# Optimization experiments

Measured on AMD Instinct MI355X. Metric: run time of the kernel, lower is better.

## Reference

```python
import jax, jax.numpy as jnp
import numpy as np

B, S, D = 2, 2048, 2048
H = 16
HD = D // H  # 128

def setup_inputs() -> dict:
    key = jax.random.key(0)
    k1, k2, k3 = jax.random.split(key, 3)
    x = jax.random.normal(k1, (B, S, D), dtype=jnp.float32)
    w_qkv = jax.random.normal(k2, (D, 3 * D), dtype=jnp.float32) * (1.0 / np.sqrt(D))
    b_qkv = jnp.zeros((3 * D,), dtype=jnp.float32)
    w_out = jax.random.normal(k3, (D, D), dtype=jnp.float32) * (1.0 / np.sqrt(D))
    b_out = jnp.zeros((D,), dtype=jnp.float32)
    return {"x": x, "w_qkv": w_qkv, "b_qkv": b_qkv, "w_out": w_out, "b_out": b_out}

def reference(x, w_qkv, b_qkv, w_out, b_out):
    batch, seq_len, channels = x.shape
    qkv = x @ w_qkv + b_qkv                      # [B,S,3D]
    q, k, v = jnp.split(qkv, 3, axis=-1)
    # [B,S,D] -> [B,H,S,HD]
    def heads(t):
        return t.reshape(batch, seq_len, H, HD).transpose(0, 2, 1, 3)
    q, k, v = heads(q), heads(k), heads(v)
    scale = 1.0 / np.sqrt(HD).astype(np.float32)
    attn = jnp.einsum('bhqd,bhkd->bhqk', q, k) * scale
    causal = jnp.tril(jnp.ones((seq_len, seq_len), dtype=bool))
    attn = jnp.where(causal, attn, -jnp.inf)
    attn = jax.nn.softmax(attn, axis=-1)
    y = jnp.einsum('bhqk,bhkd->bhqd', attn, v)   # [B,H,S,HD]
    y = y.transpose(0, 2, 1, 3).reshape(batch, seq_len, channels)
    return y @ w_out + b_out
```

## Files before the change

### kernel.cpp

```cpp
#include <hip/hip_runtime.h>
#include <hip/hip_bf16.h>
#include <cstdint>
#include <cstddef>

#define BB 2
#define SS 2048
#define DD 2048
#define HH 16
#define HDIM 128
#define QSCALE 0.12751743f

typedef short bf16x8 __attribute__((ext_vector_type(8)));
typedef float f32x4 __attribute__((ext_vector_type(4)));
typedef float f32x16 __attribute__((ext_vector_type(16)));

__device__ __forceinline__ ushort f2bf(float f) {
    union { float f; uint32_t u; } v; v.f = f;
    uint32_t u = v.u;
    u += 0x7fffu + ((u >> 16) & 1u);
    return (ushort)(u >> 16);
}

__device__ __forceinline__ ushort f2bf_fast(float f) {
    union { float f; uint32_t u; } v; v.f = f;
    return (ushort)((v.u + 0x8000u) >> 16);
}

__device__ __forceinline__ void gl16(const ushort* g, ushort* l) {
    __builtin_amdgcn_global_load_lds(
        (const __attribute__((address_space(1))) unsigned int*)g,
        (__attribute__((address_space(3))) unsigned int*)l,
        16, 0, 0);
}

__global__ __launch_bounds__(256) void cast_x_kernel(
    const float* __restrict__ X, ushort* __restrict__ Xb)
{
    size_t idx = ((size_t)blockIdx.x * 256 + threadIdx.x) * 8;
    float4 a = *(const float4*)(X + idx);
    float4 b = *(const float4*)(X + idx + 4);
    ushort4 o0, o1;
    o0.x = f2bf(a.x); o0.y = f2bf(a.y); o0.z = f2bf(a.z); o0.w = f2bf(a.w);
    o1.x = f2bf(b.x); o1.y = f2bf(b.y); o1.z = f2bf(b.z); o1.w = f2bf(b.w);
    *(ushort4*)(Xb + idx) = o0;
    *(ushort4*)(Xb + idx + 4) = o1;
}

__global__ __launch_bounds__(256) void transpose_cast_kernel(
    const float* __restrict__ W, ushort* __restrict__ Wt, int K, int N)
{
    __shared__ ushort tile[32][36];
    const int n0 = blockIdx.x * 32;
    const int k0 = blockIdx.y * 32;
    const int t = threadIdx.x;
    const int r = t >> 3;
    const int c = (t & 7) * 4;
    float4 a = *(const float4*)(W + (size_t)(k0 + r) * N + n0 + c);
    tile[r][c + 0] = f2bf(a.x); tile[r][c + 1] = f2bf(a.y);
    tile[r][c + 2] = f2bf(a.z); tile[r][c + 3] = f2bf(a.w);
    __syncthreads();
    ushort4 o;
    o.x = tile[c + 0][r]; o.y = tile[c + 1][r];
    o.z = tile[c + 2][r]; o.w = tile[c + 3][r];
    *(ushort4*)(Wt + (size_t)(n0 + r) * K + k0 + c) = o;
}

__global__ __launch_bounds__(256) void transpose_v_kernel(
    const ushort* __restrict__ V, ushort* __restrict__ Vt)
{
    __shared__ ushort tile[32][36];
    const int s0 = blockIdx.x * 32;
    const int h0 = blockIdx.y * 32;
    const int bh = blockIdx.z;
    const ushort* Vp = V + (size_t)bh * SS * HDIM;
    ushort* Vtp = Vt + (size_t)bh * HDIM * SS;
    const int t = threadIdx.x;
    const int r = t >> 3;
    const int c = (t & 7) * 4;
    *(ushort4*)&tile[r][c] = *(const ushort4*)(Vp + (size_t)(s0 + r) * HDIM + h0 + c);
    __syncthreads();
    ushort4 o;
    o.x = tile[c + 0][r]; o.y = tile[c + 1][r];
    o.z = tile[c + 2][r]; o.w = tile[c + 3][r];
    *(ushort4*)(Vtp + (size_t)(h0 + r) * SS + s0 + c) = o;
}

#define NTK 32

__global__ __launch_bounds__(512) void gemm_qkv_kernel(
    const ushort* __restrict__ A, const ushort* __restrict__ Bt,
    const float* __restrict__ bias,
    ushort* __restrict__ Qo, ushort* __restrict__ Ko, ushort* __restrict__ Vo)
{
    const int bid = blockIdx.x;
    const int wgid = (bid & 7) * 48 + (bid >> 3);
    const int mt = wgid / 24;
    const int nt = wgid - mt * 24;
    const int m0 = mt * 256, n0 = nt * 256;

    __shared__ ushort As[2][2][8192];
    __shared__ ushort Bs[2][2][8192];

    const int tid = threadIdx.x;
    const int w = tid >> 6, lane = tid & 63;
    const int wr = w >> 2, wc = w & 3;
    const int l15 = lane & 15, l4x = lane >> 4, l7 = lane & 7;

    const int rt  = w * 8 + (lane >> 3);
    const int giA = (lane & 7) ^ (lane >> 3);
    const size_t aoff = (size_t)(m0 + rt) * DD + giA * 8;
    const int nb = (w >> 2) * 64 + (w & 3) * 8 + (lane >> 3);
    const size_t boff = (size_t)(n0 + nb) * DD + giA * 8;
    const int ldst = w * 512;

    const int rdA = (wr * 64 + l15) << 7;
    const int rdB = (wc * 32 + l15) << 7;
    const int cb0 = (l4x ^ l7) << 4;
    const int cb1 = ((l4x ^ l7) ^ 4) << 4;

#define STAGE_A(t, qm) do { \
    gl16(A + aoff + (size_t)((qm) * 64) * DD + (t) * 64,       &As[(t) & 1][qm][ldst]); \
    gl16(A + aoff + (size_t)(128 + (qm) * 64) * DD + (t) * 64, &As[(t) & 1][qm][4096 + ldst]); \
} while (0)
#define STAGE_B(t, qn) do { \
    gl16(Bt + boff + (size_t)((qn) * 32) * DD + (t) * 64,       &Bs[(t) & 1][qn][ldst]); \
    gl16(Bt + boff + (size_t)(128 + (qn) * 32) * DD + (t) * 64, &Bs[(t) & 1][qn][4096 + ldst]); \
} while (0)
#define MFMA(d, x, y) d = __builtin_amdgcn_mfma_f32_16x16x32_bf16(x, y, d, 0, 0, 0)

    f32x4 acc[8][4];
#pragma unroll
    for (int i = 0; i < 8; ++i)
#pragma unroll
        for (int j = 0; j < 4; ++j) acc[i][j] = (f32x4)0.f;

    bf16x8 a[4][2], b0[2][2], b1[2][2];

    STAGE_A(0, 0); STAGE_B(0, 1); STAGE_B(0, 0); STAGE_A(0, 1);
    STAGE_A(1, 0); STAGE_B(1, 1);
    asm volatile("s_waitcnt vmcnt(4)" ::: "memory");
    __builtin_amdgcn_s_barrier();

#pragma unroll 1
    for (int t = 0; t < NTK; ++t) {
        const char* Ab = (const char*)As + (t & 1) * 32768;
        const char* Bb = (const char*)Bs + (t & 1) * 32768;

#pragma unroll
        for (int mf = 0; mf < 4; ++mf) {
            a[mf][0] = *(const bf16x8*)(Ab + rdA + mf * 2048 + cb0);
            a[mf][1] = *(const bf16x8*)(Ab + rdA + mf * 2048 + cb1);
        }
#pragma unroll
        for (int nf = 0; nf < 2; ++nf) {
            b0[nf][0] = *(const bf16x8*)(Bb + rdB + nf * 2048 + cb0);
            b0[nf][1] = *(const bf16x8*)(Bb + rdB + nf * 2048 + cb1);
        }
        if (t + 1 < NTK) STAGE_B(t + 1, 0);
        __builtin_amdgcn_s_barrier();
        asm volatile("s_waitcnt lgkmcnt(0)" ::: "memory");
        __builtin_amdgcn_s_setprio(1);
#pragma unroll
        for (int mf = 0; mf < 4; ++mf)
#pragma unroll
            for (int nf = 0; nf < 2; ++nf) {
                MFMA(acc[mf][nf], a[mf][0], b0[nf][0]);
                MFMA(acc[mf][nf], a[mf][1], b0[nf][1]);
            }
        __builtin_amdgcn_s_setprio(0);
        __builtin_amdgcn_s_barrier();

#pragma unroll
        for (int nf = 0; nf < 2; ++nf) {
            b1[nf][0] = *(const bf16x8*)(Bb + 16384 + rdB + nf * 2048 + cb0);
            b1[nf][1] = *(const bf16x8*)(Bb + 16384 + rdB + nf * 2048 + cb1);
        }
        if (t + 1 < NTK) STAGE_A(t + 1, 1);
        __builtin_amdgcn_s_barrier();
        asm volatile("s_waitcnt lgkmcnt(0)" ::: "memory");
        __builtin_amdgcn_s_setprio(1);
#pragma unroll
        for (int mf = 0; mf < 4; ++mf)
#pragma unroll
            for (int nf = 0; nf < 2; ++nf) {
                MFMA(acc[mf][2 + nf], a[mf][0], b1[nf][0]);
                MFMA(acc[mf][2 + nf], a[mf][1], b1[nf][1]);
            }
        __builtin_amdgcn_s_setprio(0);
        __builtin_amdgcn_s_barrier();

#pragma unroll
        for (int mf = 0; mf < 4; ++mf) {
            a[mf][0] = *(const bf16x8*)(Ab + 16384 + rdA + mf * 2048 + cb0);
            a[mf][1] = *(const bf16x8*)(Ab + 16384 + rdA + mf * 2048 + cb1);
        }
        if (t + 2 < NTK) STAGE_A(t + 2, 0);
        __builtin_amdgcn_s_barrier();
        asm volatile("s_waitcnt lgkmcnt(0)" ::: "memory");
        __builtin_amdgcn_s_setprio(1);
#pragma unroll
        for (int mf = 0; mf < 4; ++mf)
#pragma unroll
            for (int nf = 0; nf < 2; ++nf) {
                MFMA(acc[4 + mf][2 + nf], a[mf][0], b1[nf][0]);
                MFMA(acc[4 + mf][2 + nf], a[mf][1], b1[nf][1]);
            }
        __builtin_amdgcn_s_setprio(0);
        __builtin_amdgcn_s_barrier();

        if (t + 2 < NTK) STAGE_B(t + 2, 1);
        __builtin_amdgcn_s_barrier();
        __builtin_amdgcn_s_setprio(1);
#pragma unroll
        for (int mf = 0; mf < 4; ++mf)
#pragma unroll
            for (int nf = 0; nf < 2; ++nf) {
                MFMA(acc[4 + mf][nf], a[mf][0], b0[nf][0]);
                MFMA(acc[4 + mf][nf], a[mf][1], b0[nf][1]);
            }
        __builtin_amdgcn_s_setprio(0);
        if (t + 2 < NTK)      { asm volatile("s_waitcnt vmcnt(4)" ::: "memory"); }
        else if (t + 1 < NTK) { asm volatile("s_waitcnt vmcnt(0)" ::: "memory"); }
        __builtin_amdgcn_s_barrier();
    }
#undef STAGE_A
#undef STAGE_B
#undef MFMA

    const int which = n0 >> 11;
    ushort* dst = (which == 0) ? Qo : ((which == 1) ? Ko : Vo);
    const float sc = (which == 0) ? QSCALE : 1.0f;
    const int bidx = m0 >> 11;
    const int srow = (m0 & 2047) + wr * 128 + l4x * 4;
#pragma unroll
    for (int NF = 0; NF < 4; ++NF) {
        int n = n0 + wc * 64 + NF * 16 + l15;
        int cch = n & 2047;
        int h = cch >> 7, hd = cch & 127;
        float bv = bias[n];
        size_t base = ((size_t)(bidx * HH + h) * SS) * HDIM + hd;
#pragma unroll
        for (int MF = 0; MF < 8; ++MF) {
#pragma unroll
            for (int r = 0; r < 4; ++r) {
                int s = srow + MF * 16 + r;
                dst[base + (size_t)s * HDIM] = f2bf((acc[MF][NF][r] + bv) * sc);
            }
        }
    }
}

__global__ __launch_bounds__(256) void gemm_out_kernel(
    const ushort* __restrict__ A, const ushort* __restrict__ Bt,
    const float* __restrict__ bias, float* __restrict__ Out)
{
    const int n0 = blockIdx.x * 128;
    const int m0 = blockIdx.y * 128;
    __shared__ ushort As[128 * 32];
    __shared__ ushort Bs[128 * 32];
    const int t = threadIdx.x, w = t >> 6, lane = t & 63;
    const int l31 = lane & 31, hh = lane >> 5;
    const int lrow = lane >> 2, lks = lane & 3;
    const int wr = w >> 1, wc = w & 1;
    const int swst = (lrow >> 1) & 3;
    const int swr  = (l31 >> 1) & 3;

    f32x16 acc[2][2];
#pragma unroll
    for (int i = 0; i < 2; ++i)
#pragma unroll
        for (int j = 0; j < 2; ++j) acc[i][j] = (f32x16)0.f;

    for (int k0 = 0; k0 < DD; k0 += 32) {
        __syncthreads();
#pragma unroll
        for (int q = 0; q < 2; ++q) {
            int e = w * 2 + q;
            int row = e * 16 + lrow;
            gl16(A  + (size_t)(m0 + row) * DD + k0 + (lks ^ swst) * 8, &As[e * 512]);
            gl16(Bt + (size_t)(n0 + row) * DD + k0 + (lks ^ swst) * 8, &Bs[e * 512]);
        }
        __syncthreads();
#pragma unroll
        for (int k16 = 0; k16 < 2; ++k16) {
            int co = ((k16 * 2 + hh) ^ swr) * 8;
            bf16x8 ar0 = *(const bf16x8*)&As[(wr * 64 + l31) * 32 + co];
            bf16x8 ar1 = *(const bf16x8*)&As[(wr * 64 + 32 + l31) * 32 + co];
            bf16x8 br0 = *(const bf16x8*)&Bs[(wc * 64 + l31) * 32 + co];
            bf16x8 br1 = *(const bf16x8*)&Bs[(wc * 64 + 32 + l31) * 32 + co];
            acc[0][0] = __builtin_amdgcn_mfma_f32_32x32x16_bf16(ar0, br0, acc[0][0], 0, 0, 0);
            acc[0][1] = __builtin_amdgcn_mfma_f32_32x32x16_bf16(ar0, br1, acc[0][1], 0, 0, 0);
            acc[1][0] = __builtin_amdgcn_mfma_f32_32x32x16_bf16(ar1, br0, acc[1][0], 0, 0, 0);
            acc[1][1] = __builtin_amdgcn_mfma_f32_32x32x16_bf16(ar1, br1, acc[1][1], 0, 0, 0);
        }
    }

#pragma unroll
    for (int j = 0; j < 2; ++j) {
        int n = n0 + wc * 64 + j * 32 + l31;
        float bv = bias[n];
#pragma unroll
        for (int i = 0; i < 2; ++i) {
#pragma unroll
            for (int r = 0; r < 16; ++r) {
                int m = m0 + wr * 64 + i * 32 + (r & 3) + 8 * (r >> 2) + 4 * hh;
                Out[(size_t)m * DD + n] = acc[i][j][r] + bv;
            }
        }
    }
}

__global__ __launch_bounds__(256, 2) void attn_mfma_kernel(
    const ushort* __restrict__ Q, const ushort* __restrict__ K,
    const ushort* __restrict__ Vt, ushort* __restrict__ Y)
{
    const int bh = blockIdx.y;
    const int qt = gridDim.x - 1 - blockIdx.x;
    const int q0 = qt * 128;
    const int b = bh >> 4, h = bh & 15;

    __shared__ ushort Ks[4 * 64 * 32];
    __shared__ ushort Vs[2 * 128 * 32];
    __shared__ ushort Ps[128 * 32];

    const int t = threadIdx.x, w = t >> 6, lane = t & 63;
    const int l31 = lane & 31, hh = lane >> 5;
    const int lrow = lane >> 2, lks = lane & 3;
    const int swst = (lrow >> 1) & 3;
    const int swr  = (l31 >> 1) & 3;

    const ushort* Qp = Q  + (size_t)bh * SS * HDIM;
    const ushort* Kp = K  + (size_t)bh * SS * HDIM;
    const ushort* Vp = Vt + (size_t)bh * HDIM * SS;

    bf16x8 aq[8];
#pragma unroll
    for (int kb2 = 0; kb2 < 8; ++kb2)
        aq[kb2] = *(const bf16x8*)(Qp + (size_t)(q0 + w * 32 + l31) * HDIM + kb2 * 16 + hh * 8);

    bf16x8 ones;
#pragma unroll
    for (int j = 0; j < 8; ++j) ones[j] = (short)0x3F80;

    f32x16 O[4];
#pragma unroll
    for (int nt = 0; nt < 4; ++nt) O[nt] = (f32x16)0.f;
    f32x16 Ol = (f32x16)0.f;

    const int kbdiag = 2 * qt + (w >> 1);
    const int nkb = 2 * qt + 2;

    for (int kb = 0; kb < nkb; ++kb) {
        const int kbase = kb * 64;
        __syncthreads();
#pragma unroll
        for (int g = 0; g < 4; ++g) {
            int key = g * 16 + lrow;
            gl16(Kp + (size_t)(kbase + key) * HDIM + w * 32 + (lks ^ swst) * 8,
                 &Ks[w * 2048 + g * 512]);
        }
#pragma unroll
        for (int g = 0; g < 4; ++g) {
            int pan = g >> 1, sub = g & 1;
            int dim = w * 32 + sub * 16 + lrow;
            gl16(Vp + (size_t)dim * SS + kbase + pan * 32 + (lks ^ swst) * 8,
                 &Vs[pan * 4096 + (w * 32 + sub * 16) * 32]);
        }
        __syncthreads();

        const bool active = (kb <= kbdiag);
        if (active) {
            f32x16 sc0 = (f32x16)0.f, sc1 = (f32x16)0.f;
#pragma unroll
            for (int kb2 = 0; kb2 < 8; ++kb2) {
                int co = (((kb2 & 1) * 2 + hh) ^ swr) * 8;
                bf16x8 bk0 = *(const bf16x8*)&Ks[(kb2 >> 1) * 2048 + l31 * 32 + co];
                bf16x8 bk1 = *(const bf16x8*)&Ks[(kb2 >> 1) * 2048 + (32 + l31) * 32 + co];
                sc0 = __builtin_amdgcn_mfma_f32_32x32x16_bf16(aq[kb2], bk0, sc0, 0, 0, 0);
                sc1 = __builtin_amdgcn_mfma_f32_32x32x16_bf16(aq[kb2], bk1, sc1, 0, 0, 0);
            }

            if (kb == kbdiag) {
#pragma unroll
                for (int r = 0; r < 16; ++r) {
                    int rowg = q0 + w * 32 + (r & 3) + 8 * (r >> 2) + 4 * hh;
                    if (kbase + l31 > rowg)      sc0[r] = -1e30f;
                    if (kbase + 32 + l31 > rowg) sc1[r] = -1e30f;
                }
            }

#pragma unroll
            for (int half = 0; half < 2; ++half) {
#pragma unroll
                for (int r = 0; r < 16; ++r) {
                    float sv = (half == 0) ? sc0[r] : sc1[r];
                    float p = __builtin_amdgcn_exp2f(sv);
                    int rowm = (r & 3) + 8 * (r >> 2) + 4 * hh;
                    int pc = (l31 >> 3) ^ ((rowm >> 1) & 3);
                    Ps[(w * 32 + rowm) * 32 + (pc << 3) + (l31 & 7)] = f2bf_fast(p);
                }
#pragma unroll
                for (int kblk2 = 0; kblk2 < 2; ++kblk2) {
                    int co = ((kblk2 * 2 + hh) ^ swr) * 8;
                    bf16x8 ap = *(const bf16x8*)&Ps[(w * 32 + l31) * 32 + co];
#pragma unroll
                    for (int nt = 0; nt < 4; ++nt) {
                        bf16x8 bv = *(const bf16x8*)&Vs[half * 4096 + (nt * 32 + l31) * 32 + co];
                        O[nt] = __builtin_amdgcn_mfma_f32_32x32x16_bf16(ap, bv, O[nt], 0, 0, 0);
                    }
                    Ol = __builtin_amdgcn_mfma_f32_32x32x16_bf16(ap, ones, Ol, 0, 0, 0);
                }
            }
        }
    }

#pragma unroll
    for (int r = 0; r < 16; ++r) {
        int s = q0 + w * 32 + (r & 3) + 8 * (r >> 2) + 4 * hh;
        float inv = 1.0f / Ol[r];
        size_t base = ((size_t)(b * SS + s)) * DD + h * HDIM;
#pragma unroll
        for (int nt = 0; nt < 4; ++nt)
            Y[base + nt * 32 + l31] = f2bf(O[nt][r] * inv);
    }
}

extern "C" void kernel_launch(void* const* d_in, const int* in_sizes, int n_in,
                              void* d_out, int out_size, void* d_ws, size_t ws_size,
                              hipStream_t stream) {
    const float* x     = (const float*)d_in[0];
    const float* w_qkv = (const float*)d_in[1];
    const float* b_qkv = (const float*)d_in[2];
    const float* w_out = (const float*)d_in[3];
    const float* b_out = (const float*)d_in[4];
    float* out = (float*)d_out;

    ushort* ws  = (ushort*)d_ws;
    ushort* xb  = ws;
    ushort* wtq = xb + 8388608;
    ushort* wto = wtq + 12582912;
    ushort* q   = wto + 4194304;
    ushort* k   = q + 8388608;
    ushort* v   = k + 8388608;
    ushort* vt  = v + 8388608;
    ushort* y   = vt + 8388608;

    cast_x_kernel<<<4096, 256, 0, stream>>>(x, xb);
    transpose_cast_kernel<<<dim3(192, 64), 256, 0, stream>>>(w_qkv, wtq, DD, 3 * DD);
    transpose_cast_kernel<<<dim3(64, 64), 256, 0, stream>>>(w_out, wto, DD, DD);
    gemm_qkv_kernel<<<384, 512, 0, stream>>>(xb, wtq, b_qkv, q, k, v);
    transpose_v_kernel<<<dim3(64, 4, 32), 256, 0, stream>>>(v, vt);
    attn_mfma_kernel<<<dim3(16, 32), 256, 0, stream>>>(q, k, vt, y);
    gemm_out_kernel<<<dim3(16, 32), 256, 0, stream>>>(y, wto, b_out, out);
}
```

Before: 400.4 us.

## Collapse four-phase GEMM main loop into two phases with one-tile prefetch

```diff
diff --git a/kernel.cpp b/kernel.cpp
--- a/kernel.cpp
+++ b/kernel.cpp
@@ -136,9 +136,9 @@
 
     bf16x8 a[4][2], b0[2][2], b1[2][2];
 
-    STAGE_A(0, 0); STAGE_B(0, 1); STAGE_B(0, 0); STAGE_A(0, 1);
-    STAGE_A(1, 0); STAGE_B(1, 1);
-    asm volatile("s_waitcnt vmcnt(4)" ::: "memory");
+    STAGE_A(0, 0); STAGE_B(0, 0); STAGE_B(0, 1);
+    STAGE_A(0, 1);
+    asm volatile("s_waitcnt vmcnt(2)" ::: "memory");
     __builtin_amdgcn_s_barrier();
 
 #pragma unroll 1
@@ -146,6 +146,7 @@
         const char* Ab = (const char*)As + (t & 1) * 32768;
         const char* Bb = (const char*)Bs + (t & 1) * 32768;
 
+        if (t + 1 < NTK) { STAGE_B(t + 1, 0); STAGE_B(t + 1, 1); STAGE_A(t + 1, 0); }
 #pragma unroll
         for (int mf = 0; mf < 4; ++mf) {
             a[mf][0] = *(const bf16x8*)(Ab + rdA + mf * 2048 + cb0);
@@ -155,8 +156,11 @@
         for (int nf = 0; nf < 2; ++nf) {
             b0[nf][0] = *(const bf16x8*)(Bb + rdB + nf * 2048 + cb0);
             b0[nf][1] = *(const bf16x8*)(Bb + rdB + nf * 2048 + cb1);
-        }
-        if (t + 1 < NTK) STAGE_B(t + 1, 0);
+            b1[nf][0] = *(const bf16x8*)(Bb + 16384 + rdB + nf * 2048 + cb0);
+            b1[nf][1] = *(const bf16x8*)(Bb + 16384 + rdB + nf * 2048 + cb1);
+        }
+        if (t + 1 < NTK) { asm volatile("s_waitcnt vmcnt(6)" ::: "memory"); }
+        else             { asm volatile("s_waitcnt vmcnt(0)" ::: "memory"); }
         __builtin_amdgcn_s_barrier();
         asm volatile("s_waitcnt lgkmcnt(0)" ::: "memory");
         __builtin_amdgcn_s_setprio(1);
@@ -166,16 +170,18 @@
             for (int nf = 0; nf < 2; ++nf) {
                 MFMA(acc[mf][nf], a[mf][0], b0[nf][0]);
                 MFMA(acc[mf][nf], a[mf][1], b0[nf][1]);
+                MFMA(acc[mf][2 + nf], a[mf][0], b1[nf][0]);
+                MFMA(acc[mf][2 + nf], a[mf][1], b1[nf][1]);
             }
         __builtin_amdgcn_s_setprio(0);
-        __builtin_amdgcn_s_barrier();
-
-#pragma unroll
-        for (int nf = 0; nf < 2; ++nf) {
-            b1[nf][0] = *(const bf16x8*)(Bb + 16384 + rdB + nf * 2048 + cb0);
-            b1[nf][1] = *(const bf16x8*)(Bb + 16384 + rdB + nf * 2048 + cb1);
-        }
+
         if (t + 1 < NTK) STAGE_A(t + 1, 1);
+#pragma unroll
+        for (int mf = 0; mf < 4; ++mf) {
+            a[mf][0] = *(const bf16x8*)(Ab + 16384 + rdA + mf * 2048 + cb0);
+            a[mf][1] = *(const bf16x8*)(Ab + 16384 + rdA + mf * 2048 + cb1);
+        }
+        asm volatile("s_waitcnt vmcnt(2)" ::: "memory");
         __builtin_amdgcn_s_barrier();
         asm volatile("s_waitcnt lgkmcnt(0)" ::: "memory");
         __builtin_amdgcn_s_setprio(1);
@@ -183,45 +189,12 @@
         for (int mf = 0; mf < 4; ++mf)
 #pragma unroll
             for (int nf = 0; nf < 2; ++nf) {
-                MFMA(acc[mf][2 + nf], a[mf][0], b1[nf][0]);
-                MFMA(acc[mf][2 + nf], a[mf][1], b1[nf][1]);
-            }
-        __builtin_amdgcn_s_setprio(0);
-        __builtin_amdgcn_s_barrier();
-
-#pragma unroll
-        for (int mf = 0; mf < 4; ++mf) {
-            a[mf][0] = *(const bf16x8*)(Ab + 16384 + rdA + mf * 2048 + cb0);
-            a[mf][1] = *(const bf16x8*)(Ab + 16384 + rdA + mf * 2048 + cb1);
-        }
-        if (t + 2 < NTK) STAGE_A(t + 2, 0);
-        __builtin_amdgcn_s_barrier();
-        asm volatile("s_waitcnt lgkmcnt(0)" ::: "memory");
-        __builtin_amdgcn_s_setprio(1);
-#pragma unroll
-        for (int mf = 0; mf < 4; ++mf)
-#pragma unroll
-            for (int nf = 0; nf < 2; ++nf) {
+                MFMA(acc[4 + mf][nf], a[mf][0], b0[nf][0]);
+                MFMA(acc[4 + mf][nf], a[mf][1], b0[nf][1]);
                 MFMA(acc[4 + mf][2 + nf], a[mf][0], b1[nf][0]);
                 MFMA(acc[4 + mf][2 + nf], a[mf][1], b1[nf][1]);
             }
         __builtin_amdgcn_s_setprio(0);
-        __builtin_amdgcn_s_barrier();
-
-        if (t + 2 < NTK) STAGE_B(t + 2, 1);
-        __builtin_amdgcn_s_barrier();
-        __builtin_amdgcn_s_setprio(1);
-#pragma unroll
-        for (int mf = 0; mf < 4; ++mf)
-#pragma unroll
-            for (int nf = 0; nf < 2; ++nf) {
-                MFMA(acc[4 + mf][nf], a[mf][0], b0[nf][0]);
-                MFMA(acc[4 + mf][nf], a[mf][1], b0[nf][1]);
-            }
-        __builtin_amdgcn_s_setprio(0);
-        if (t + 2 < NTK)      { asm volatile("s_waitcnt vmcnt(4)" ::: "memory"); }
-        else if (t + 1 < NTK) { asm volatile("s_waitcnt vmcnt(0)" ::: "memory"); }
-        __builtin_amdgcn_s_barrier();
     }
 #undef STAGE_A
 #undef STAGE_B
```

Result: slower. 437.7 us (+9.3%).
